# Kernel tuning notes

Measured on AMD Instinct MI355X. Metric: run time of the kernel, lower is better.

## Reference

```python
import jax, jax.numpy as jnp
import numpy as np

H = 256


def _lstm_cell(inp, hx, cx, Wih, Whh, bih, bhh):
    # PyTorch LSTMCell: gate order i, f, g, o
    gates = inp @ Wih.T + bih + hx @ Whh.T + bhh
    i, f, g, o = jnp.split(gates, 4, axis=-1)
    c = jax.nn.sigmoid(f) * cx + jax.nn.sigmoid(i) * jnp.tanh(g)
    h = jax.nn.sigmoid(o) * jnp.tanh(c)
    return h, c


def _match(p_enc, q_enc, wq, wp, whr_w, whr_b, w_vec, w_b0, Wih, Whh, bih, bhh, reverse):
    # p_enc: (P,B,H) time-major passage; q_enc, wq: (Q,B,H); wp: (P,B,H)
    B = p_enc.shape[1]

    def step(carry, xs):
        hx, cx = carry
        wphp, p_t = xs                                  # (B,H), (B,H)
        wrhr = hx @ whr_w.T + whr_b                     # (B,H)
        g = jnp.tanh(wq + (wphp + wrhr))                # (Q,B,H)
        scores = jnp.einsum('qbh,h->bq', g, w_vec) + w_b0
        alpha = jax.nn.softmax(scores, axis=-1)         # (B,Q)
        attn = jnp.einsum('bq,qbh->bh', alpha, q_enc)   # (B,H)
        inp = jnp.concatenate([p_t, attn], axis=-1)     # (B,2H)
        hx, cx = _lstm_cell(inp, hx, cx, Wih, Whh, bih, bhh)
        return (hx, cx), hx

    init = (jnp.zeros((B, H), p_enc.dtype), jnp.zeros((B, H), p_enc.dtype))
    _, hs = jax.lax.scan(step, init, (wp, p_enc), reverse=reverse)
    return hs  # (P,B,H), always in natural time order


def setup_inputs() -> dict:
    key = jax.random.key(0)
    ks = jax.random.split(key, 20)
    s = 0.05
    return {
        'passage': jax.random.normal(ks[0], (64, 512, H), jnp.float32),
        'question': jax.random.normal(ks[1], (64, 64, H), jnp.float32),
        'whq_w': jax.random.normal(ks[2], (H, H), jnp.float32) * s,
        'whq_b': jax.random.normal(ks[3], (H,), jnp.float32) * s,
        'whp_w': jax.random.normal(ks[4], (H, H), jnp.float32) * s,
        'whp_b': jax.random.normal(ks[5], (H,), jnp.float32) * s,
        'whr_w': jax.random.normal(ks[6], (H, H), jnp.float32) * s,
        'whr_b': jax.random.normal(ks[7], (H,), jnp.float32) * s,
        'w_w': jax.random.normal(ks[8], (1, H), jnp.float32) * s,
        'w_b': jax.random.normal(ks[9], (1,), jnp.float32) * s,
        'fw_Wih': jax.random.normal(ks[10], (4 * H, 2 * H), jnp.float32) * s,
        'fw_Whh': jax.random.normal(ks[11], (4 * H, H), jnp.float32) * s,
        'fw_bih': jax.random.normal(ks[12], (4 * H,), jnp.float32) * s,
        'fw_bhh': jax.random.normal(ks[13], (4 * H,), jnp.float32) * s,
        'bw_Wih': jax.random.normal(ks[14], (4 * H, 2 * H), jnp.float32) * s,
        'bw_Whh': jax.random.normal(ks[15], (4 * H, H), jnp.float32) * s,
        'bw_bih': jax.random.normal(ks[16], (4 * H,), jnp.float32) * s,
        'bw_bhh': jax.random.normal(ks[17], (4 * H,), jnp.float32) * s,
    }


def reference(passage, question, whq_w, whq_b, whp_w, whp_b, whr_w, whr_b,
              w_w, w_b, fw_Wih, fw_Whh, fw_bih, fw_bhh,
              bw_Wih, bw_Whh, bw_bih, bw_bhh):
    p = jnp.swapaxes(passage, 0, 1)    # (P,B,H)
    q = jnp.swapaxes(question, 0, 1)   # (Q,B,H)
    wq = q @ whq_w.T + whq_b           # (Q,B,H)  (dropout p=0.0 -> identity)
    wp = p @ whp_w.T + whp_b           # (P,B,H)
    fw = _match(p, q, wq, wp, whr_w, whr_b, w_w[0], w_b[0],
                fw_Wih, fw_Whh, fw_bih, fw_bhh, reverse=False)
    bw = _match(p, q, wq, wp, whr_w, whr_b, w_w[0], w_b[0],
                bw_Wih, bw_Whh, bw_bih, bw_bhh, reverse=True)
    return jnp.concatenate([fw, bw], axis=-1)  # (P,B,2H)
```

## Files before the change

### kernel.cpp

```cpp
#include <hip/hip_runtime.h>

#define HN 256
#define QN 64
#define PN 512
#define CH 8

typedef float f4 __attribute__((ext_vector_type(4)));

__device__ __forceinline__ float dot4(f4 a, f4 b) {
  return a.x * b.x + a.y * b.y + a.z * b.z + a.w * b.w;
}
__device__ __forceinline__ float fast_sig(float x) {
  return __builtin_amdgcn_rcpf(1.f + __builtin_amdgcn_exp2f(-1.44269504f * x));
}
__device__ __forceinline__ float fast_tanh(float x) {
  return 1.f - 2.f * __builtin_amdgcn_rcpf(1.f + __builtin_amdgcn_exp2f(2.88539008f * x));
}

struct SMem {
  union {
    float q32[QN][HN];
    struct {
      alignas(16) float pgc[CH][1024];
      alignas(16) float wpc[CH][HN];
      alignas(16) float pch[CH][HN];
    } c;
  } u;
  alignas(16) float hx[HN];
  float cx[HN];
  alignas(16) float wA[HN];
  float wrb[HN];
  float gates[1024];
  float scores[QN];
  alignas(16) float al[QN];
};
static_assert(sizeof(SMem) <= 160 * 1024, "LDS overflow");

__global__ void __launch_bounds__(1024, 1)
match_kernel(const float* __restrict__ passage, const float* __restrict__ question,
             const float* __restrict__ whq_w, const float* __restrict__ whq_b,
             const float* __restrict__ whp_w, const float* __restrict__ whp_b,
             const float* __restrict__ whr_w, const float* __restrict__ whr_b,
             const float* __restrict__ w_w,
             const float* __restrict__ Wih_f, const float* __restrict__ Whh_f,
             const float* __restrict__ bih_f, const float* __restrict__ bhh_f,
             const float* __restrict__ Wih_b, const float* __restrict__ Whh_b,
             const float* __restrict__ bih_b, const float* __restrict__ bhh_b,
             float* __restrict__ out)
{
  __shared__ SMem sm;
  const int t = threadIdx.x;
  const int bid = blockIdx.x;
  const int e = bid & 7;
  const int dir = e >> 2;
  const int b = ((bid >> 3) << 2) | (e & 3);

  const float* Wih = dir ? Wih_b : Wih_f;
  const float* Whh = dir ? Whh_b : Whh_f;
  const float* bih = dir ? bih_b : bih_f;
  const float* bhh = dir ? bhh_b : bhh_f;

  const int qB = t >> 4;
  const int sg = t & 15;
  const int g2 = t >> 4;

  {
    const int q = t >> 4, c0 = (t & 15) * 16;
    const float* src = question + ((size_t)b * QN + q) * HN + c0;
    #pragma unroll
    for (int m = 0; m < 4; ++m)
      *(f4*)&sm.u.q32[q][c0 + 4 * m] = *(const f4*)(src + 4 * m);
  }
  if (t < HN) { sm.hx[t] = 0.f; sm.cx[t] = 0.f; sm.wrb[t] = whr_b[t]; }
  __syncthreads();

  float wqr[16], wwr[16];
  #pragma unroll
  for (int j = 0; j < 16; ++j) {
    wqr[j] = whq_b[sg * 16 + j];
    wwr[j] = w_w[sg * 16 + j];
  }
  for (int k = 0; k < HN; k += 4) {
    f4 qv = *(const f4*)&sm.u.q32[qB][k];
    #pragma unroll
    for (int j = 0; j < 16; ++j) {
      f4 w = *(const f4*)(whq_w + (size_t)(sg * 16 + j) * HN + k);
      wqr[j] += dot4(w, qv);
    }
  }

  float gq[QN];
  #pragma unroll
  for (int q = 0; q < QN; ++q) gq[q] = 0.f;
  {
    const float* wrow = Wih + (size_t)t * 512 + 256;
    for (int i = 0; i < 64; ++i) {
      f4 w = *(const f4*)(wrow + 4 * i);
      #pragma unroll
      for (int q = 0; q < QN; ++q)
        gq[q] += dot4(w, *(const f4*)&sm.u.q32[q][4 * i]);
    }
  }
  const float biasr = bih[t] + bhh[t];
  __syncthreads();

  const int tb = dir ? (PN - 1) : 0;
  const int ts = dir ? -1 : 1;

  for (int s = 0; s < PN; ++s) {
    const int tau = s & (CH - 1);
    if (tau == 0) {
      if (t < 512) {
        const int tt = t >> 6, cc = (t & 63) * 4;
        const int trow = tb + ts * (s + tt);
        *(f4*)&sm.u.c.pch[tt][cc] =
            *(const f4*)(passage + ((size_t)b * PN + trow) * HN + cc);
      }
      __syncthreads();
      #pragma unroll
      for (int rr = 0; rr < 4; ++rr) {
        const int h = g2 + 64 * rr;
        const float* wrow = whp_w + (size_t)h * HN + sg * 4;
        float acc[CH];
        #pragma unroll
        for (int uu = 0; uu < CH; ++uu) acc[uu] = 0.f;
        #pragma unroll
        for (int m = 0; m < 4; ++m) {
          f4 w = *(const f4*)(wrow + m * 64);
          #pragma unroll
          for (int uu = 0; uu < CH; ++uu)
            acc[uu] += dot4(w, *(const f4*)&sm.u.c.pch[uu][m * 64 + sg * 4]);
        }
        #pragma unroll
        for (int uu = 0; uu < CH; ++uu) {
          acc[uu] += __shfl_xor(acc[uu], 1);
          acc[uu] += __shfl_xor(acc[uu], 2);
          acc[uu] += __shfl_xor(acc[uu], 4);
          acc[uu] += __shfl_xor(acc[uu], 8);
        }
        if (sg == rr) {
          const float pb = whp_b[h];
          #pragma unroll
          for (int uu = 0; uu < CH; ++uu) sm.u.c.wpc[uu][h] = acc[uu] + pb;
        }
      }
      #pragma unroll
      for (int rr = 0; rr < 16; ++rr) {
        const int r = g2 + 64 * rr;
        const float* wrow = Wih + (size_t)r * 512 + sg * 4;
        float acc[CH];
        #pragma unroll
        for (int uu = 0; uu < CH; ++uu) acc[uu] = 0.f;
        #pragma unroll
        for (int m = 0; m < 4; ++m) {
          f4 w = *(const f4*)(wrow + m * 64);
          #pragma unroll
          for (int uu = 0; uu < CH; ++uu)
            acc[uu] += dot4(w, *(const f4*)&sm.u.c.pch[uu][m * 64 + sg * 4]);
        }
        #pragma unroll
        for (int uu = 0; uu < CH; ++uu) {
          acc[uu] += __shfl_xor(acc[uu], 1);
          acc[uu] += __shfl_xor(acc[uu], 2);
          acc[uu] += __shfl_xor(acc[uu], 4);
          acc[uu] += __shfl_xor(acc[uu], 8);
        }
        if (sg == rr) {
          #pragma unroll
          for (int uu = 0; uu < CH; ++uu) sm.u.c.pgc[uu][r] = acc[uu];
        }
      }
      __syncthreads();
    }

    #pragma unroll
    for (int rr = 0; rr < 4; ++rr) {
      const int h = g2 + 64 * rr;
      const float* wrow = whr_w + (size_t)h * HN + sg * 4;
      float a = 0.f;
      #pragma unroll
      for (int m = 0; m < 4; ++m)
        a += dot4(*(const f4*)(wrow + m * 64),
                  *(const f4*)&sm.hx[m * 64 + sg * 4]);
      a += __shfl_xor(a, 1);
      a += __shfl_xor(a, 2);
      a += __shfl_xor(a, 4);
      a += __shfl_xor(a, 8);
      if (sg == rr) sm.wA[h] = a + sm.u.c.wpc[tau][h] + sm.wrb[h];
    }
    __syncthreads();

    {
      float sc = 0.f;
      #pragma unroll
      for (int jj = 0; jj < 4; ++jj) {
        f4 a4 = *(const f4*)&sm.wA[sg * 16 + 4 * jj];
        sc += fast_tanh(wqr[4 * jj + 0] + a4.x) * wwr[4 * jj + 0];
        sc += fast_tanh(wqr[4 * jj + 1] + a4.y) * wwr[4 * jj + 1];
        sc += fast_tanh(wqr[4 * jj + 2] + a4.z) * wwr[4 * jj + 2];
        sc += fast_tanh(wqr[4 * jj + 3] + a4.w) * wwr[4 * jj + 3];
      }
      sc += __shfl_xor(sc, 1);
      sc += __shfl_xor(sc, 2);
      sc += __shfl_xor(sc, 4);
      sc += __shfl_xor(sc, 8);
      if (sg == 0) sm.scores[qB] = sc;
    }
    __syncthreads();

    #pragma unroll
    for (int rr = 0; rr < 16; ++rr) {
      const int r = g2 + 64 * rr;
      const float* wrow = Whh + (size_t)r * HN + sg * 4;
      float a = 0.f;
      #pragma unroll
      for (int m = 0; m < 4; ++m)
        a += dot4(*(const f4*)(wrow + m * 64),
                  *(const f4*)&sm.hx[m * 64 + sg * 4]);
      a += __shfl_xor(a, 1);
      a += __shfl_xor(a, 2);
      a += __shfl_xor(a, 4);
      a += __shfl_xor(a, 8);
      if (sg == rr) sm.gates[r] = a;
    }
    if (t < 64) {
      float sv = sm.scores[t];
      float mx = sv;
      #pragma unroll
      for (int o = 1; o < 64; o <<= 1) mx = fmaxf(mx, __shfl_xor(mx, o));
      float ex = __builtin_amdgcn_exp2f(1.44269504f * (sv - mx));
      float sum = ex;
      #pragma unroll
      for (int o = 1; o < 64; o <<= 1) sum += __shfl_xor(sum, o);
      sm.al[t] = ex * __builtin_amdgcn_rcpf(sum);
    }
    __syncthreads();

    {
      float acc = sm.gates[t] + sm.u.c.pgc[tau][t] + biasr;
      #pragma unroll
      for (int jj = 0; jj < 16; ++jj) {
        f4 av = *(const f4*)&sm.al[4 * jj];
        acc += gq[4 * jj + 0] * av.x + gq[4 * jj + 1] * av.y
             + gq[4 * jj + 2] * av.z + gq[4 * jj + 3] * av.w;
      }
      sm.gates[t] = acc;
    }
    __syncthreads();

    if (t < HN) {
      float gi = sm.gates[t], gf = sm.gates[HN + t];
      float gg = sm.gates[2 * HN + t], go = sm.gates[3 * HN + t];
      float c = fast_sig(gf) * sm.cx[t] + fast_sig(gi) * fast_tanh(gg);
      float hn = fast_sig(go) * fast_tanh(c);
      sm.cx[t] = c;
      sm.hx[t] = hn;
      const int trow = tb + ts * s;
      out[((size_t)trow * 64 + b) * 512 + dir * HN + t] = hn;
    }
    __syncthreads();
  }
}

extern "C" void kernel_launch(void* const* d_in, const int* in_sizes, int n_in,
                              void* d_out, int out_size, void* d_ws, size_t ws_size,
                              hipStream_t stream) {
  (void)in_sizes; (void)n_in; (void)out_size; (void)d_ws; (void)ws_size;
  match_kernel<<<dim3(128), dim3(1024), 0, stream>>>(
      (const float*)d_in[0],
      (const float*)d_in[1],
      (const float*)d_in[2],
      (const float*)d_in[3],
      (const float*)d_in[4],
      (const float*)d_in[5],
      (const float*)d_in[6],
      (const float*)d_in[7],
      (const float*)d_in[8],
      (const float*)d_in[10],
      (const float*)d_in[11],
      (const float*)d_in[12],
      (const float*)d_in[13],
      (const float*)d_in[14],
      (const float*)d_in[15],
      (const float*)d_in[16],
      (const float*)d_in[17],
      (float*)d_out);
}
```

Measured before the change: 28.99 ms.

## Move wq projection to LDS and relax launch bounds to cut register pressure

```diff
diff --git a/kernel.cpp b/kernel.cpp
--- a/kernel.cpp
+++ b/kernel.cpp
@@ -26,6 +26,8 @@
       alignas(16) float pch[CH][HN];
     } c;
   } u;
+  alignas(16) float wqt[QN][HN + 4];
+  alignas(16) float ww[HN];
   alignas(16) float hx[HN];
   float cx[HN];
   alignas(16) float wA[HN];
@@ -35,8 +37,9 @@
   alignas(16) float al[QN];
 };
 static_assert(sizeof(SMem) <= 160 * 1024, "LDS overflow");
-
-__global__ void __launch_bounds__(1024, 1)
+static_assert(sizeof(SMem) > 80 * 1024, "want exactly 1 block/CU");
+
+__global__ void __launch_bounds__(1024, 4)
 match_kernel(const float* __restrict__ passage, const float* __restrict__ question,
              const float* __restrict__ whq_w, const float* __restrict__ whq_b,
              const float* __restrict__ whp_w, const float* __restrict__ whp_b,
@@ -71,22 +74,29 @@
     for (int m = 0; m < 4; ++m)
       *(f4*)&sm.u.q32[q][c0 + 4 * m] = *(const f4*)(src + 4 * m);
   }
-  if (t < HN) { sm.hx[t] = 0.f; sm.cx[t] = 0.f; sm.wrb[t] = whr_b[t]; }
+  if (t < HN) {
+    sm.hx[t] = 0.f; sm.cx[t] = 0.f;
+    sm.wrb[t] = whr_b[t]; sm.ww[t] = w_w[t];
+  }
   __syncthreads();
 
-  float wqr[16], wwr[16];
-  #pragma unroll
-  for (int j = 0; j < 16; ++j) {
-    wqr[j] = whq_b[sg * 16 + j];
-    wwr[j] = w_w[sg * 16 + j];
-  }
-  for (int k = 0; k < HN; k += 4) {
-    f4 qv = *(const f4*)&sm.u.q32[qB][k];
-    #pragma unroll
-    for (int j = 0; j < 16; ++j) {
-      f4 w = *(const f4*)(whq_w + (size_t)(sg * 16 + j) * HN + k);
-      wqr[j] += dot4(w, qv);
-    }
+  {
+    const int h = t & 255, qh = (t >> 8) * 16;
+    float acc[16];
+    const float qb = whq_b[h];
+    #pragma unroll
+    for (int i2 = 0; i2 < 16; ++i2) acc[i2] = qb;
+    const float* wrow = whq_w + (size_t)h * HN;
+    for (int k = 0; k < HN; k += 4) {
+      f4 w4 = *(const f4*)(wrow + k);
+      #pragma unroll
+      for (int i2 = 0; i2 < 16; ++i2) {
+        f4 qv = *(const f4*)&sm.u.q32[qh + i2][k];
+        acc[i2] += dot4(w4, qv);
+      }
+    }
+    #pragma unroll
+    for (int i2 = 0; i2 < 16; ++i2) sm.wqt[qh + i2][h] = acc[i2];
   }
 
   float gq[QN];
@@ -195,10 +205,12 @@
       #pragma unroll
       for (int jj = 0; jj < 4; ++jj) {
         f4 a4 = *(const f4*)&sm.wA[sg * 16 + 4 * jj];
-        sc += fast_tanh(wqr[4 * jj + 0] + a4.x) * wwr[4 * jj + 0];
-        sc += fast_tanh(wqr[4 * jj + 1] + a4.y) * wwr[4 * jj + 1];
-        sc += fast_tanh(wqr[4 * jj + 2] + a4.z) * wwr[4 * jj + 2];
-        sc += fast_tanh(wqr[4 * jj + 3] + a4.w) * wwr[4 * jj + 3];
+        f4 q4 = *(const f4*)&sm.wqt[qB][sg * 16 + 4 * jj];
+        f4 w4 = *(const f4*)&sm.ww[sg * 16 + 4 * jj];
+        sc += fast_tanh(q4.x + a4.x) * w4.x;
+        sc += fast_tanh(q4.y + a4.y) * w4.y;
+        sc += fast_tanh(q4.z + a4.z) * w4.z;
+        sc += fast_tanh(q4.w + a4.w) * w4.w;
       }
       sc += __shfl_xor(sc, 1);
       sc += __shfl_xor(sc, 2);
```

Result: faster. 27.62 ms (-4.7%).
